# Kernel tuning notes

Measured on AMD Instinct MI355X. Metric: run time of the kernel, lower is better.

Reference implementation:

```python
import jax, jax.numpy as jnp
import numpy as np

B, S, D_IN, H = 64, 512, 2, 512


def lstm_cell(x, h, c, Wih, Whh, b):
    # PyTorch nn.LSTM gate layout: [i, f, g, o] stacked along rows of W (4H x in)
    gates = x @ Wih.T + h @ Whh.T + b  # [B, 4H]
    i, f, g, o = jnp.split(gates, 4, axis=-1)
    c = jax.nn.sigmoid(f) * c + jax.nn.sigmoid(i) * jnp.tanh(g)
    h = jax.nn.sigmoid(o) * jnp.tanh(c)
    return h, c


def setup_inputs() -> dict:
    key = jax.random.key(0)
    ks = jax.random.split(key, 12)
    s = 1.0 / np.sqrt(H)  # torch default uniform init scale
    u = lambda k, shape: jax.random.uniform(k, shape, jnp.float32, -s, s)
    return {
        "inputs": jax.random.normal(ks[0], (B, S, D_IN), jnp.float32),
        "enc_Wih": u(ks[1], (4 * H, D_IN)),
        "enc_Whh": u(ks[2], (4 * H, H)),
        "enc_bih": u(ks[3], (4 * H,)),
        "enc_bhh": u(ks[4], (4 * H,)),
        "dec_Wih": u(ks[5], (4 * H, H)),
        "dec_Whh": u(ks[6], (4 * H, H)),
        "dec_bih": u(ks[7], (4 * H,)),
        "dec_bhh": u(ks[8], (4 * H,)),
        "W_key": u(ks[9], (H, H)),
        "W_query": u(ks[10], (H, H)),
        "v": u(ks[11], (H,)),
        "max_output_len": S,
    }


def reference(inputs, enc_Wih, enc_Whh, enc_bih, enc_bhh,
              dec_Wih, dec_Whh, dec_bih, dec_bhh,
              W_key, W_query, v, max_output_len):
    batch, seq_len, _ = inputs.shape
    hid = W_key.shape[0]
    dtype = inputs.dtype

    # ---- Encoder LSTM over the sequence ----
    enc_b = enc_bih + enc_bhh
    h0 = jnp.zeros((batch, hid), dtype)

    def enc_step(carry, x_t):
        h, c = carry
        h, c = lstm_cell(x_t, h, c, enc_Wih, enc_Whh, enc_b)
        return (h, c), h

    (h, c), enc_outs = jax.lax.scan(enc_step, (h0, h0), jnp.swapaxes(inputs, 0, 1))
    enc_outs = jnp.swapaxes(enc_outs, 0, 1)  # [B, S, H]

    # keys are recomputed each step in the torch code but are step-invariant
    keys = enc_outs @ W_key.T  # [B, S, H]
    dec_b = dec_bih + dec_bhh

    # ---- Decoder loop with Bahdanau pointer attention ----
    def dec_step(carry, _):
        h_d, c_d, x = carry
        h_d, c_d = lstm_cell(x, h_d, c_d, dec_Wih, dec_Whh, dec_b)
        query = h_d @ W_query.T                                # [B, H]
        scores = jnp.tanh(query[:, None, :] + keys) @ v        # [B, S]
        probs = jax.nn.softmax(scores, axis=-1)
        context = jnp.einsum('bs,bsh->bh', probs, enc_outs)    # [B, H]
        return (h_d, c_d, context), scores

    x0 = jnp.zeros((batch, hid), dtype)
    _, all_scores = jax.lax.scan(dec_step, (h, c, x0), None, length=max_output_len)
    return jnp.swapaxes(all_scores, 0, 1)  # [B, T, S]
```

## Files before the change

### kernel.cpp

```cpp
#include <hip/hip_runtime.h>

constexpr int kNB = 64;
constexpr int kNS = 512;
constexpr int kNH = 512;
constexpr int kNG = 2048;
constexpr int kNT = 512;

__device__ __forceinline__ float chpn_sigmoid(float x) {
    return 1.0f / (1.0f + __expf(-x));
}
__device__ __forceinline__ float chpn_tanh(float x) {
    x = fmaxf(fminf(x, 15.0f), -15.0f);
    float e = __expf(2.0f * x);
    return (e - 1.0f) / (e + 1.0f);
}

__global__ void ConvexHullPointerNetwork_57303453663418_kernel(
    const float* ebih, const float* ebhh,
    const float* dbih, const float* dbhh,
    const float* wq,
    float* enc_b, float* dec_b, float* wqT, float* h0c)
{
    int i = blockIdx.x * 256 + threadIdx.x;
    if (i < kNG) { enc_b[i] = ebih[i] + ebhh[i]; dec_b[i] = dbih[i] + dbhh[i]; }
    if (i < 2 * kNB * kNH) h0c[i] = 0.0f;
    if (i < kNH * kNH) {
        int r = i >> 9, c = i & 511;
        wqT[c * kNH + r] = wq[i];
    }
}

__global__ __launch_bounds__(256) void chpn_enc_cell(
    const float* __restrict__ inputs, const float* __restrict__ wih,
    const float* __restrict__ whh, const float* __restrict__ bias,
    const float* __restrict__ h_src, float* __restrict__ h_dst,
    float* __restrict__ c_st, float* __restrict__ enc_outs, int t)
{
    __shared__ float tile[64][65];
    __shared__ float gate_lds[4][64];
    const int tid = threadIdx.x;
    const int bb = tid & 63, gg = tid >> 6;
    const int j = (int)blockIdx.x;

    const int r = gg * kNH + j;
    const float* w = whh + (size_t)r * kNH;
    float acc = 0.f;

    for (int ch = 0; ch < 8; ++ch) {
        const int k0 = ch * 64;
        for (int i = 0; i < 16; ++i) {
            int e = tid + i * 256; int kk = e & 63, b2 = e >> 6;
            tile[kk][b2] = h_src[b2 * kNH + k0 + kk];
        }
        __syncthreads();
        #pragma unroll
        for (int kk = 0; kk < 64; ++kk)
            acc = fmaf(tile[kk][bb], w[k0 + kk], acc);
        __syncthreads();
    }
    float x0 = inputs[(bb * kNS + t) * 2 + 0];
    float x1 = inputs[(bb * kNS + t) * 2 + 1];
    acc += bias[r] + wih[r * 2] * x0 + wih[r * 2 + 1] * x1;

    gate_lds[gg][bb] = acc;
    __syncthreads();
    if (tid < 64) {
        float gi = gate_lds[0][tid], gf = gate_lds[1][tid];
        float gc = gate_lds[2][tid], go = gate_lds[3][tid];
        float cc = chpn_sigmoid(gf) * c_st[tid * kNH + j] + chpn_sigmoid(gi) * chpn_tanh(gc);
        float hh = chpn_sigmoid(go) * chpn_tanh(cc);
        c_st[tid * kNH + j] = cc;
        h_dst[tid * kNH + j] = hh;
        enc_outs[((size_t)tid * kNS + t) * kNH + j] = hh;
    }
}

__global__ __launch_bounds__(256) void chpn_keys_gemm(
    const float* __restrict__ enc_outs, const float* __restrict__ wk,
    float* __restrict__ keysT)
{
    int bid = blockIdx.x;
    int bb = bid >> 6, ht = (bid >> 3) & 7, st = bid & 7;
    __shared__ float asb[32][66];
    __shared__ float bsb[32][66];
    int tid = threadIdx.x;
    int tx = tid & 15, ty = tid >> 4;
    float acc[4][4] = {};
    for (int j0 = 0; j0 < kNH; j0 += 32) {
        for (int i = 0; i < 8; ++i) {
            int e = tid + i * 256;
            int j = e & 31, s = e >> 5;
            asb[j][s] = enc_outs[((size_t)bb * kNS + st * 64 + s) * kNH + j0 + j];
            bsb[j][s] = wk[(size_t)(ht * 64 + s) * kNH + j0 + j];
        }
        __syncthreads();
        #pragma unroll 8
        for (int j = 0; j < 32; ++j) {
            float a0 = asb[j][tx*4], a1 = asb[j][tx*4+1], a2 = asb[j][tx*4+2], a3 = asb[j][tx*4+3];
            float b0 = bsb[j][ty*4], b1 = bsb[j][ty*4+1], b2 = bsb[j][ty*4+2], b3 = bsb[j][ty*4+3];
            acc[0][0] = fmaf(b0,a0,acc[0][0]); acc[0][1] = fmaf(b0,a1,acc[0][1]);
            acc[0][2] = fmaf(b0,a2,acc[0][2]); acc[0][3] = fmaf(b0,a3,acc[0][3]);
            acc[1][0] = fmaf(b1,a0,acc[1][0]); acc[1][1] = fmaf(b1,a1,acc[1][1]);
            acc[1][2] = fmaf(b1,a2,acc[1][2]); acc[1][3] = fmaf(b1,a3,acc[1][3]);
            acc[2][0] = fmaf(b2,a0,acc[2][0]); acc[2][1] = fmaf(b2,a1,acc[2][1]);
            acc[2][2] = fmaf(b2,a2,acc[2][2]); acc[2][3] = fmaf(b2,a3,acc[2][3]);
            acc[3][0] = fmaf(b3,a0,acc[3][0]); acc[3][1] = fmaf(b3,a1,acc[3][1]);
            acc[3][2] = fmaf(b3,a2,acc[3][2]); acc[3][3] = fmaf(b3,a3,acc[3][3]);
        }
        __syncthreads();
    }
    for (int i = 0; i < 4; ++i)
        for (int k = 0; k < 4; ++k)
            keysT[((size_t)bb * kNH + ht * 64 + ty * 4 + i) * kNS + st * 64 + tx * 4 + k] =
                acc[i][k];
}

__global__ __launch_bounds__(256) void chpn_dec_cell(
    const float* __restrict__ wih, const float* __restrict__ whh,
    const float* __restrict__ bias,
    const float* __restrict__ h_src, float* __restrict__ h_dst,
    float* __restrict__ c_st,
    const float* __restrict__ ctx_num, const float* __restrict__ denom,
    int first)
{
    __shared__ float tile[64][65];
    __shared__ float gate_lds[4][64];
    __shared__ float invd[64];
    const int tid = threadIdx.x;
    const int bb = tid & 63, gg = tid >> 6;
    const int j = (int)blockIdx.x;
    if (tid < 64) invd[tid] = first ? 0.0f : (1.0f / denom[tid]);
    __syncthreads();

    const int r = gg * kNH + j;
    float acc = 0.f;
    {
        const float* w = wih + (size_t)r * kNH;
        for (int ch = 0; ch < 8; ++ch) {
            const int k0 = ch * 64;
            for (int i = 0; i < 16; ++i) {
                int e = tid + i * 256; int kk = e & 63, b2 = e >> 6;
                tile[kk][b2] = first ? 0.0f : ctx_num[b2 * kNH + k0 + kk] * invd[b2];
            }
            __syncthreads();
            #pragma unroll
            for (int kk = 0; kk < 64; ++kk)
                acc = fmaf(tile[kk][bb], w[k0 + kk], acc);
            __syncthreads();
        }
    }
    {
        const float* w = whh + (size_t)r * kNH;
        for (int ch = 0; ch < 8; ++ch) {
            const int k0 = ch * 64;
            for (int i = 0; i < 16; ++i) {
                int e = tid + i * 256; int kk = e & 63, b2 = e >> 6;
                tile[kk][b2] = h_src[b2 * kNH + k0 + kk];
            }
            __syncthreads();
            #pragma unroll
            for (int kk = 0; kk < 64; ++kk)
                acc = fmaf(tile[kk][bb], w[k0 + kk], acc);
            __syncthreads();
        }
    }
    acc += bias[r];
    gate_lds[gg][bb] = acc;
    __syncthreads();
    if (tid < 64) {
        float gi = gate_lds[0][tid], gf = gate_lds[1][tid];
        float gc = gate_lds[2][tid], go = gate_lds[3][tid];
        float cc = chpn_sigmoid(gf) * c_st[tid * kNH + j] + chpn_sigmoid(gi) * chpn_tanh(gc);
        float hh = chpn_sigmoid(go) * chpn_tanh(cc);
        c_st[tid * kNH + j] = cc;
        h_dst[tid * kNH + j] = hh;
    }
}

__global__ __launch_bounds__(256) void chpn_query(
    const float* __restrict__ wqT, const float* __restrict__ h_src,
    float* __restrict__ query, float* __restrict__ ctx_num,
    float* __restrict__ denom)
{
    __shared__ float hl[kNH];
    __shared__ float part[256];
    int bid = blockIdx.x;
    int bb = bid >> 2, hc = bid & 3;
    int tid = threadIdx.x;
    int hl_idx = tid;
    hl[hl_idx] = h_src[bb * kNH + hl_idx];
    hl[hl_idx + 256] = h_src[bb * kNH + hl_idx + 256];
    __syncthreads();

    int h = hc * 128 + (tid & 127);
    int jh = tid >> 7;
    float acc = 0.f;
    const float* wcol = wqT + h;
    #pragma unroll 8
    for (int j = jh * 256; j < jh * 256 + 256; ++j)
        acc = fmaf(hl[j], wcol[(size_t)j * kNH], acc);
    part[tid] = acc;
    __syncthreads();
    if (tid < 128) {
        float q = part[tid] + part[tid + 128];
        query[bb * kNH + h] = q;
        ctx_num[bb * kNH + h] = 0.0f;
        if (hc == 0 && tid == 0) denom[bb] = 0.0f;
    }
}

__global__ __launch_bounds__(1024) void chpn_score_ctx(
    const float* __restrict__ keysT, const float* __restrict__ enc_outs,
    const float* __restrict__ query, const float* __restrict__ vvec,
    float* __restrict__ ctx_num, float* __restrict__ denom,
    float* __restrict__ out, int t)
{
    __shared__ float ql[kNH], vl[kNH];
    __shared__ float part[16][64];
    __shared__ float el[64];
    int bid = blockIdx.x;
    int bb = bid >> 3, sc = bid & 7;
    int s0 = sc * 64;
    int tid = threadIdx.x;
    int s = tid & 63, hq = tid >> 6;

    if (tid < kNH) { ql[tid] = query[bb * kNH + tid]; vl[tid] = vvec[tid]; }
    __syncthreads();

    float acc = 0.f;
    const float* kp = keysT + (size_t)bb * kNH * kNS + s0 + s;
    const int h0 = hq * 32;
    #pragma unroll 4
    for (int h = h0; h < h0 + 32; ++h) {
        float kv = kp[(size_t)h * kNS];
        acc = fmaf(vl[h], chpn_tanh(ql[h] + kv), acc);
    }
    part[hq][s] = acc;
    __syncthreads();

    if (tid < 64) {
        float scv = 0.f;
        #pragma unroll
        for (int q = 0; q < 16; ++q) scv += part[q][tid];
        out[((size_t)bb * kNT + t) * kNS + s0 + tid] = scv;
        float e = __expf(scv);
        el[tid] = e;
        float wsum = e;
        #pragma unroll
        for (int off = 32; off > 0; off >>= 1) wsum += __shfl_down(wsum, off);
        if (tid == 0) atomicAdd(&denom[bb], wsum);
    }
    __syncthreads();

    int j = tid & 511, sh = tid >> 9;
    float a = 0.f;
    const float* ep = enc_outs + ((size_t)bb * kNS + s0 + sh * 32) * kNH + j;
    #pragma unroll 4
    for (int ss = 0; ss < 32; ++ss)
        a = fmaf(el[sh * 32 + ss], ep[(size_t)ss * kNH], a);
    atomicAdd(&ctx_num[bb * kNH + j], a);
}

extern "C" void kernel_launch(void* const* d_in, const int* in_sizes, int n_in,
                              void* d_out, int out_size, void* d_ws, size_t ws_size,
                              hipStream_t stream) {
    const float* inputs = (const float*)d_in[0];
    const float* e_wih  = (const float*)d_in[1];
    const float* e_whh  = (const float*)d_in[2];
    const float* e_bih  = (const float*)d_in[3];
    const float* e_bhh  = (const float*)d_in[4];
    const float* d_wih  = (const float*)d_in[5];
    const float* d_whh  = (const float*)d_in[6];
    const float* d_bih  = (const float*)d_in[7];
    const float* d_bhh  = (const float*)d_in[8];
    const float* w_key  = (const float*)d_in[9];
    const float* w_qry  = (const float*)d_in[10];
    const float* v_vec  = (const float*)d_in[11];
    float* out = (float*)d_out;

    float* wsf   = (float*)d_ws;
    float* h0    = wsf;
    float* cst   = h0 + kNB * kNH;
    float* h1    = cst + kNB * kNH;
    float* query = h1 + kNB * kNH;
    float* ctxn  = query + kNB * kNH;
    float* denom = ctxn + kNB * kNH;
    float* encb  = denom + 64;
    float* decb  = encb + kNG;
    float* wqT   = decb + kNG;
    float* keysF = wqT + (size_t)kNH * kNH;
    float* encF  = keysF + (size_t)kNB * kNH * kNS;

    ConvexHullPointerNetwork_57303453663418_kernel<<<1024, 256, 0, stream>>>(
        e_bih, e_bhh, d_bih, d_bhh, w_qry, encb, decb, wqT, h0);

    for (int t = 0; t < kNS; ++t) {
        float* hs = (t & 1) ? h1 : h0;
        float* hd = (t & 1) ? h0 : h1;
        chpn_enc_cell<<<512, 256, 0, stream>>>(inputs, e_wih, e_whh, encb,
                                               hs, hd, cst, encF, t);
    }

    chpn_keys_gemm<<<4096, 256, 0, stream>>>(encF, w_key, keysF);

    for (int t = 0; t < kNT; ++t) {
        float* hs = (t & 1) ? h1 : h0;
        float* hd = (t & 1) ? h0 : h1;
        chpn_dec_cell<<<512, 256, 0, stream>>>(d_wih, d_whh, decb,
                                               hs, hd, cst,
                                               ctxn, denom, t == 0 ? 1 : 0);
        chpn_query<<<256, 256, 0, stream>>>(wqT, hd, query, ctxn, denom);
        chpn_score_ctx<<<512, 1024, 0, stream>>>(keysF, encF, query, v_vec,
                                                 ctxn, denom, out, t);
    }
}
```

Measured before the change: 70.88 ms.

## Replace per-step launches with persistent per-batch encoder and decoder loop kernels

Replaces the 512 encoder launches and 1536 decoder launches with two persistent kernels, one 1024-thread block per batch row, that keep h, c, context and softmax state in shared memory across all timesteps. Weights are pre-transposed so each thread streams coalesced gate rows every step. Encoder outputs and keys are stored as fp16 to halve attention traffic. This removes launch overhead, global state round-trips and atomics, but uses only 64 blocks on a large GPU and re-reads the full weight matrices from cache every step, with some fp16 precision loss.

```diff
diff --git a/kernel.cpp b/kernel.cpp
--- a/kernel.cpp
+++ b/kernel.cpp
@@ -6,6 +6,8 @@
 constexpr int kNG = 2048;
 constexpr int kNT = 512;
 
+typedef _Float16 chpn_f16;
+
 __device__ __forceinline__ float chpn_sigmoid(float x) {
     return 1.0f / (1.0f + __expf(-x));
 }
@@ -18,66 +20,87 @@
 __global__ void ConvexHullPointerNetwork_57303453663418_kernel(
     const float* ebih, const float* ebhh,
     const float* dbih, const float* dbhh,
-    const float* wq,
-    float* enc_b, float* dec_b, float* wqT, float* h0c)
+    const float* ewhh, const float* dwih, const float* dwhh, const float* wq,
+    float* enc_b, float* dec_b, float* weT, float* wdT, float* wqT)
 {
-    int i = blockIdx.x * 256 + threadIdx.x;
-    if (i < kNG) { enc_b[i] = ebih[i] + ebhh[i]; dec_b[i] = dbih[i] + dbhh[i]; }
-    if (i < 2 * kNB * kNH) h0c[i] = 0.0f;
-    if (i < kNH * kNH) {
-        int r = i >> 9, c = i & 511;
-        wqT[c * kNH + r] = wq[i];
-    }
-}
-
-__global__ __launch_bounds__(256) void chpn_enc_cell(
+    size_t i = (size_t)blockIdx.x * 256 + threadIdx.x;
+    size_t stride = (size_t)gridDim.x * 256;
+    for (size_t x = i; x < (size_t)kNG; x += stride) {
+        enc_b[x] = ebih[x] + ebhh[x];
+        dec_b[x] = dbih[x] + dbhh[x];
+    }
+    for (size_t x = i; x < (size_t)kNH * kNG; x += stride) {
+        size_t k = x / kNG, r = x % kNG;
+        weT[x] = ewhh[r * kNH + k];
+    }
+    for (size_t x = i; x < (size_t)2 * kNH * kNG; x += stride) {
+        size_t k = x / kNG, r = x % kNG;
+        wdT[x] = (k < kNH) ? dwih[r * kNH + k] : dwhh[r * kNH + (k - kNH)];
+    }
+    for (size_t x = i; x < (size_t)kNH * kNH; x += stride) {
+        size_t j = x / kNH, h = x % kNH;
+        wqT[x] = wq[h * kNH + j];
+    }
+}
+
+__global__ __launch_bounds__(1024) void chpn_enc_loop(
     const float* __restrict__ inputs, const float* __restrict__ wih,
-    const float* __restrict__ whh, const float* __restrict__ bias,
-    const float* __restrict__ h_src, float* __restrict__ h_dst,
-    float* __restrict__ c_st, float* __restrict__ enc_outs, int t)
+    const float* __restrict__ weT, const float* __restrict__ bias,
+    float* __restrict__ hfin, float* __restrict__ cfin,
+    chpn_f16* __restrict__ enc_outs)
 {
-    __shared__ float tile[64][65];
-    __shared__ float gate_lds[4][64];
+    __shared__ float h_l[kNH];
+    __shared__ float c_l[kNH];
+    __shared__ float gates[kNG];
     const int tid = threadIdx.x;
-    const int bb = tid & 63, gg = tid >> 6;
-    const int j = (int)blockIdx.x;
-
-    const int r = gg * kNH + j;
-    const float* w = whh + (size_t)r * kNH;
-    float acc = 0.f;
-
-    for (int ch = 0; ch < 8; ++ch) {
-        const int k0 = ch * 64;
-        for (int i = 0; i < 16; ++i) {
-            int e = tid + i * 256; int kk = e & 63, b2 = e >> 6;
-            tile[kk][b2] = h_src[b2 * kNH + k0 + kk];
-        }
-        __syncthreads();
-        #pragma unroll
-        for (int kk = 0; kk < 64; ++kk)
-            acc = fmaf(tile[kk][bb], w[k0 + kk], acc);
-        __syncthreads();
-    }
-    float x0 = inputs[(bb * kNS + t) * 2 + 0];
-    float x1 = inputs[(bb * kNS + t) * 2 + 1];
-    acc += bias[r] + wih[r * 2] * x0 + wih[r * 2 + 1] * x1;
-
-    gate_lds[gg][bb] = acc;
+    const int b = (int)blockIdx.x;
+    const int r0 = tid, r1 = tid + 1024;
+
+    if (tid < kNH) { h_l[tid] = 0.f; c_l[tid] = 0.f; }
     __syncthreads();
-    if (tid < 64) {
-        float gi = gate_lds[0][tid], gf = gate_lds[1][tid];
-        float gc = gate_lds[2][tid], go = gate_lds[3][tid];
-        float cc = chpn_sigmoid(gf) * c_st[tid * kNH + j] + chpn_sigmoid(gi) * chpn_tanh(gc);
-        float hh = chpn_sigmoid(go) * chpn_tanh(cc);
-        c_st[tid * kNH + j] = cc;
-        h_dst[tid * kNH + j] = hh;
-        enc_outs[((size_t)tid * kNS + t) * kNH + j] = hh;
+
+    const float b0 = bias[r0], b1 = bias[r1];
+    const float w00 = wih[r0 * 2], w01 = wih[r0 * 2 + 1];
+    const float w10 = wih[r1 * 2], w11 = wih[r1 * 2 + 1];
+
+    for (int t = 0; t < kNS; ++t) {
+        float a0 = 0.f, a1 = 0.f;
+        const float* wp = weT;
+        #pragma unroll 4
+        for (int k = 0; k < kNH; ++k) {
+            float hk = h_l[k];
+            a0 = fmaf(wp[r0], hk, a0);
+            a1 = fmaf(wp[r1], hk, a1);
+            wp += kNG;
+        }
+        float x0 = inputs[(b * kNS + t) * 2 + 0];
+        float x1 = inputs[(b * kNS + t) * 2 + 1];
+        a0 += b0 + w00 * x0 + w01 * x1;
+        a1 += b1 + w10 * x0 + w11 * x1;
+        gates[r0] = a0;
+        gates[r1] = a1;
+        __syncthreads();
+        if (tid < kNH) {
+            float gi = gates[tid], gf = gates[kNH + tid];
+            float gc = gates[2 * kNH + tid], go = gates[3 * kNH + tid];
+            float cc = chpn_sigmoid(gf) * c_l[tid] +
+                       chpn_sigmoid(gi) * chpn_tanh(gc);
+            float hh = chpn_sigmoid(go) * chpn_tanh(cc);
+            c_l[tid] = cc;
+            h_l[tid] = hh;
+            enc_outs[((size_t)b * kNS + t) * kNH + tid] = (chpn_f16)hh;
+        }
+        __syncthreads();
+    }
+    if (tid < kNH) {
+        hfin[b * kNH + tid] = h_l[tid];
+        cfin[b * kNH + tid] = c_l[tid];
     }
 }
 
 __global__ __launch_bounds__(256) void chpn_keys_gemm(
-    const float* __restrict__ enc_outs, const float* __restrict__ wk,
-    float* __restrict__ keysT)
+    const chpn_f16* __restrict__ enc_outs, const float* __restrict__ wk,
+    chpn_f16* __restrict__ keysT)
 {
     int bid = blockIdx.x;
     int bb = bid >> 6, ht = (bid >> 3) & 7, st = bid & 7;
@@ -90,7 +113,7 @@
         for (int i = 0; i < 8; ++i) {
             int e = tid + i * 256;
             int j = e & 31, s = e >> 5;
-            asb[j][s] = enc_outs[((size_t)bb * kNS + st * 64 + s) * kNH + j0 + j];
+            asb[j][s] = (float)enc_outs[((size_t)bb * kNS + st * 64 + s) * kNH + j0 + j];
             bsb[j][s] = wk[(size_t)(ht * 64 + s) * kNH + j0 + j];
         }
         __syncthreads();
@@ -112,153 +135,136 @@
     for (int i = 0; i < 4; ++i)
         for (int k = 0; k < 4; ++k)
             keysT[((size_t)bb * kNH + ht * 64 + ty * 4 + i) * kNS + st * 64 + tx * 4 + k] =
-                acc[i][k];
-}
-
-__global__ __launch_bounds__(256) void chpn_dec_cell(
-    const float* __restrict__ wih, const float* __restrict__ whh,
-    const float* __restrict__ bias,
-    const float* __restrict__ h_src, float* __restrict__ h_dst,
-    float* __restrict__ c_st,
-    const float* __restrict__ ctx_num, const float* __restrict__ denom,
-    int first)
+                (chpn_f16)acc[i][k];
+}
+
+__global__ __launch_bounds__(1024) void chpn_dec_loop(
+    const float* __restrict__ wdT, const float* __restrict__ bias,
+    const float* __restrict__ wqT, const float* __restrict__ vvec,
+    const chpn_f16* __restrict__ keysT, const chpn_f16* __restrict__ enc_outs,
+    const float* __restrict__ hfin, const float* __restrict__ cfin,
+    float* __restrict__ out)
 {
-    __shared__ float tile[64][65];
-    __shared__ float gate_lds[4][64];
-    __shared__ float invd[64];
+    __shared__ float h_l[kNH];
+    __shared__ float c_l[kNH];
+    __shared__ float ctx[kNH];
+    __shared__ float gates[kNG];
+    __shared__ float q_l[kNH];
+    __shared__ float qpart[2][kNH];
+    __shared__ float vl[kNH];
+    __shared__ float el[kNS];
+    __shared__ float part[2][kNS];
+    __shared__ float cpart[2][kNH];
+    __shared__ float dpart[8];
+    __shared__ float dinv;
+
     const int tid = threadIdx.x;
-    const int bb = tid & 63, gg = tid >> 6;
-    const int j = (int)blockIdx.x;
-    if (tid < 64) invd[tid] = first ? 0.0f : (1.0f / denom[tid]);
+    const int b = (int)blockIdx.x;
+    const int r0 = tid, r1 = tid + 1024;
+    const float b0 = bias[r0], b1 = bias[r1];
+    const int half = tid >> 9;
+    const int lid = tid & 511;
+    const chpn_f16* keyb = keysT + (size_t)b * kNH * kNS;
+    const chpn_f16* encb2 = enc_outs + (size_t)b * kNS * kNH;
+
+    if (tid < kNH) {
+        h_l[tid] = hfin[b * kNH + tid];
+        c_l[tid] = cfin[b * kNH + tid];
+        ctx[tid] = 0.f;
+        vl[tid] = vvec[tid];
+    }
     __syncthreads();
 
-    const int r = gg * kNH + j;
-    float acc = 0.f;
-    {
-        const float* w = wih + (size_t)r * kNH;
-        for (int ch = 0; ch < 8; ++ch) {
-            const int k0 = ch * 64;
-            for (int i = 0; i < 16; ++i) {
-                int e = tid + i * 256; int kk = e & 63, b2 = e >> 6;
-                tile[kk][b2] = first ? 0.0f : ctx_num[b2 * kNH + k0 + kk] * invd[b2];
-            }
-            __syncthreads();
-            #pragma unroll
-            for (int kk = 0; kk < 64; ++kk)
-                acc = fmaf(tile[kk][bb], w[k0 + kk], acc);
-            __syncthreads();
-        }
-    }
-    {
-        const float* w = whh + (size_t)r * kNH;
-        for (int ch = 0; ch < 8; ++ch) {
-            const int k0 = ch * 64;
-            for (int i = 0; i < 16; ++i) {
-                int e = tid + i * 256; int kk = e & 63, b2 = e >> 6;
-                tile[kk][b2] = h_src[b2 * kNH + k0 + kk];
-            }
-            __syncthreads();
-            #pragma unroll
-            for (int kk = 0; kk < 64; ++kk)
-                acc = fmaf(tile[kk][bb], w[k0 + kk], acc);
-            __syncthreads();
-        }
-    }
-    acc += bias[r];
-    gate_lds[gg][bb] = acc;
-    __syncthreads();
-    if (tid < 64) {
-        float gi = gate_lds[0][tid], gf = gate_lds[1][tid];
-        float gc = gate_lds[2][tid], go = gate_lds[3][tid];
-        float cc = chpn_sigmoid(gf) * c_st[tid * kNH + j] + chpn_sigmoid(gi) * chpn_tanh(gc);
-        float hh = chpn_sigmoid(go) * chpn_tanh(cc);
-        c_st[tid * kNH + j] = cc;
-        h_dst[tid * kNH + j] = hh;
-    }
-}
-
-__global__ __launch_bounds__(256) void chpn_query(
-    const float* __restrict__ wqT, const float* __restrict__ h_src,
-    float* __restrict__ query, float* __restrict__ ctx_num,
-    float* __restrict__ denom)
-{
-    __shared__ float hl[kNH];
-    __shared__ float part[256];
-    int bid = blockIdx.x;
-    int bb = bid >> 2, hc = bid & 3;
-    int tid = threadIdx.x;
-    int hl_idx = tid;
-    hl[hl_idx] = h_src[bb * kNH + hl_idx];
-    hl[hl_idx + 256] = h_src[bb * kNH + hl_idx + 256];
-    __syncthreads();
-
-    int h = hc * 128 + (tid & 127);
-    int jh = tid >> 7;
-    float acc = 0.f;
-    const float* wcol = wqT + h;
-    #pragma unroll 8
-    for (int j = jh * 256; j < jh * 256 + 256; ++j)
-        acc = fmaf(hl[j], wcol[(size_t)j * kNH], acc);
-    part[tid] = acc;
-    __syncthreads();
-    if (tid < 128) {
-        float q = part[tid] + part[tid + 128];
-        query[bb * kNH + h] = q;
-        ctx_num[bb * kNH + h] = 0.0f;
-        if (hc == 0 && tid == 0) denom[bb] = 0.0f;
-    }
-}
-
-__global__ __launch_bounds__(1024) void chpn_score_ctx(
-    const float* __restrict__ keysT, const float* __restrict__ enc_outs,
-    const float* __restrict__ query, const float* __restrict__ vvec,
-    float* __restrict__ ctx_num, float* __restrict__ denom,
-    float* __restrict__ out, int t)
-{
-    __shared__ float ql[kNH], vl[kNH];
-    __shared__ float part[16][64];
-    __shared__ float el[64];
-    int bid = blockIdx.x;
-    int bb = bid >> 3, sc = bid & 7;
-    int s0 = sc * 64;
-    int tid = threadIdx.x;
-    int s = tid & 63, hq = tid >> 6;
-
-    if (tid < kNH) { ql[tid] = query[bb * kNH + tid]; vl[tid] = vvec[tid]; }
-    __syncthreads();
-
-    float acc = 0.f;
-    const float* kp = keysT + (size_t)bb * kNH * kNS + s0 + s;
-    const int h0 = hq * 32;
-    #pragma unroll 4
-    for (int h = h0; h < h0 + 32; ++h) {
-        float kv = kp[(size_t)h * kNS];
-        acc = fmaf(vl[h], chpn_tanh(ql[h] + kv), acc);
-    }
-    part[hq][s] = acc;
-    __syncthreads();
-
-    if (tid < 64) {
-        float scv = 0.f;
-        #pragma unroll
-        for (int q = 0; q < 16; ++q) scv += part[q][tid];
-        out[((size_t)bb * kNT + t) * kNS + s0 + tid] = scv;
-        float e = __expf(scv);
-        el[tid] = e;
-        float wsum = e;
-        #pragma unroll
-        for (int off = 32; off > 0; off >>= 1) wsum += __shfl_down(wsum, off);
-        if (tid == 0) atomicAdd(&denom[bb], wsum);
-    }
-    __syncthreads();
-
-    int j = tid & 511, sh = tid >> 9;
-    float a = 0.f;
-    const float* ep = enc_outs + ((size_t)bb * kNS + s0 + sh * 32) * kNH + j;
-    #pragma unroll 4
-    for (int ss = 0; ss < 32; ++ss)
-        a = fmaf(el[sh * 32 + ss], ep[(size_t)ss * kNH], a);
-    atomicAdd(&ctx_num[bb * kNH + j], a);
+    for (int t = 0; t < kNT; ++t) {
+        float a0 = 0.f, a1 = 0.f;
+        {
+            const float* wp = wdT;
+            #pragma unroll 4
+            for (int k = 0; k < kNH; ++k) {
+                float ck = ctx[k];
+                a0 = fmaf(wp[r0], ck, a0);
+                a1 = fmaf(wp[r1], ck, a1);
+                wp += kNG;
+            }
+            #pragma unroll 4
+            for (int k = 0; k < kNH; ++k) {
+                float hk = h_l[k];
+                a0 = fmaf(wp[r0], hk, a0);
+                a1 = fmaf(wp[r1], hk, a1);
+                wp += kNG;
+            }
+        }
+        a0 += b0; a1 += b1;
+        gates[r0] = a0;
+        gates[r1] = a1;
+        __syncthreads();
+        if (tid < kNH) {
+            float gi = gates[tid], gf = gates[kNH + tid];
+            float gc = gates[2 * kNH + tid], go = gates[3 * kNH + tid];
+            float cc = chpn_sigmoid(gf) * c_l[tid] +
+                       chpn_sigmoid(gi) * chpn_tanh(gc);
+            float hh = chpn_sigmoid(go) * chpn_tanh(cc);
+            c_l[tid] = cc;
+            h_l[tid] = hh;
+        }
+        __syncthreads();
+
+        {
+            float qa = 0.f;
+            const float* wp = wqT + (size_t)half * 256 * kNH + lid;
+            #pragma unroll 4
+            for (int jx = 0; jx < 256; ++jx)
+                qa = fmaf(h_l[half * 256 + jx], wp[(size_t)jx * kNH], qa);
+            qpart[half][lid] = qa;
+            __syncthreads();
+            if (tid < kNH) q_l[tid] = qpart[0][tid] + qpart[1][tid];
+            __syncthreads();
+        }
+
+        {
+            float sa = 0.f;
+            const chpn_f16* kp = keyb + (size_t)half * 256 * kNS + lid;
+            const int hb = half * 256;
+            #pragma unroll 4
+            for (int hx = 0; hx < 256; ++hx) {
+                float kv = (float)kp[(size_t)hx * kNS];
+                sa = fmaf(vl[hb + hx], chpn_tanh(q_l[hb + hx] + kv), sa);
+            }
+            part[half][lid] = sa;
+            __syncthreads();
+            if (tid < kNS) {
+                float scv = part[0][tid] + part[1][tid];
+                out[((size_t)b * kNT + t) * kNS + tid] = scv;
+                float e = __expf(scv);
+                el[tid] = e;
+                float wsum = e;
+                #pragma unroll
+                for (int off = 32; off > 0; off >>= 1)
+                    wsum += __shfl_down(wsum, off);
+                if ((tid & 63) == 0) dpart[tid >> 6] = wsum;
+            }
+            __syncthreads();
+            if (tid == 0) {
+                float d = 0.f;
+                #pragma unroll
+                for (int o = 0; o < 8; ++o) d += dpart[o];
+                dinv = 1.0f / d;
+            }
+            __syncthreads();
+        }
+
+        {
+            float ca = 0.f;
+            const chpn_f16* ep = encb2 + (size_t)half * 256 * kNH + lid;
+            #pragma unroll 4
+            for (int sx = 0; sx < 256; ++sx)
+                ca = fmaf(el[half * 256 + sx], (float)ep[(size_t)sx * kNH], ca);
+            cpart[half][lid] = ca;
+            __syncthreads();
+            if (tid < kNH) ctx[tid] = (cpart[0][tid] + cpart[1][tid]) * dinv;
+            __syncthreads();
+        }
+    }
 }
 
 extern "C" void kernel_launch(void* const* d_in, const int* in_sizes, int n_in,
@@ -279,38 +285,25 @@
     float* out = (float*)d_out;
 
     float* wsf   = (float*)d_ws;
-    float* h0    = wsf;
-    float* cst   = h0 + kNB * kNH;
-    float* h1    = cst + kNB * kNH;
-    float* query = h1 + kNB * kNH;
-    float* ctxn  = query + kNB * kNH;
-    float* denom = ctxn + kNB * kNH;
-    float* encb  = denom + 64;
+    float* encb  = wsf;
     float* decb  = encb + kNG;
     float* wqT   = decb + kNG;
-    float* keysF = wqT + (size_t)kNH * kNH;
-    float* encF  = keysF + (size_t)kNB * kNH * kNS;
-
-    ConvexHullPointerNetwork_57303453663418_kernel<<<1024, 256, 0, stream>>>(
-        e_bih, e_bhh, d_bih, d_bhh, w_qry, encb, decb, wqT, h0);
-
-    for (int t = 0; t < kNS; ++t) {
-        float* hs = (t & 1) ? h1 : h0;
-        float* hd = (t & 1) ? h0 : h1;
-        chpn_enc_cell<<<512, 256, 0, stream>>>(inputs, e_wih, e_whh, encb,
-                                               hs, hd, cst, encF, t);
-    }
-
-    chpn_keys_gemm<<<4096, 256, 0, stream>>>(encF, w_key, keysF);
-
-    for (int t = 0; t < kNT; ++t) {
-        float* hs = (t & 1) ? h1 : h0;
-        float* hd = (t & 1) ? h0 : h1;
-        chpn_dec_cell<<<512, 256, 0, stream>>>(d_wih, d_whh, decb,
-                                               hs, hd, cst,
-                                               ctxn, denom, t == 0 ? 1 : 0);
-        chpn_query<<<256, 256, 0, stream>>>(wqT, hd, query, ctxn, denom);
-        chpn_score_ctx<<<512, 1024, 0, stream>>>(keysF, encF, query, v_vec,
-                                                 ctxn, denom, out, t);
-    }
-}
+    float* weT   = wqT + (size_t)kNH * kNH;
+    float* wdT   = weT + (size_t)kNH * kNG;
+    float* hfin  = wdT + (size_t)2 * kNH * kNG;
+    float* cfin  = hfin + (size_t)kNB * kNH;
+    chpn_f16* keysH = (chpn_f16*)(cfin + (size_t)kNB * kNH);
+    chpn_f16* encH  = keysH + (size_t)kNB * kNH * kNS;
+
+    ConvexHullPointerNetwork_57303453663418_kernel<<<4096, 256, 0, stream>>>(
+        e_bih, e_bhh, d_bih, d_bhh, e_whh, d_wih, d_whh, w_qry,
+        encb, decb, weT, wdT, wqT);
+
+    chpn_enc_loop<<<64, 1024, 0, stream>>>(inputs, e_wih, weT, encb,
+                                           hfin, cfin, encH);
+
+    chpn_keys_gemm<<<4096, 256, 0, stream>>>(encH, w_key, keysH);
+
+    chpn_dec_loop<<<64, 1024, 0, stream>>>(wdT, decb, wqT, v_vec,
+                                           keysH, encH, hfin, cfin, out);
+}
```

New measurement: 114.8 ms. +62.0%, slower.
